# Optimization experiments

Measured on AMD Instinct MI355X. Metric: run time of the kernel, lower is better.

Reference implementation:

```python
import jax, jax.numpy as jnp
import numpy as np

B, S, H = 128, 1000, 256


def setup_inputs() -> dict:
    key = jax.random.key(0)
    ks = jax.random.split(key, 15)
    sc = 1.0 / np.sqrt(H)
    f = lambda k, shape: (jax.random.normal(k, shape, jnp.float32) * sc)
    return dict(
        static_hidden=jax.random.normal(ks[0], (B, S, H), jnp.float32),
        state_embedding=jax.random.normal(ks[1], (B, 1, H), jnp.float32),
        decoder_hidden=jax.random.normal(ks[2], (B, 1, H), jnp.float32),
        target_hidden=jax.random.normal(ks[3], (B, 1, H), jnp.float32),
        last_hh=jax.random.normal(ks[4], (1, B, H), jnp.float32),
        W_ih=f(ks[5], (3 * H, H)),
        W_hh=f(ks[6], (3 * H, H)),
        b_ih=f(ks[7], (3 * H,)),
        b_hh=f(ks[8], (3 * H,)),
        v_attn_enc=f(ks[9], (H,)),
        W_attn_enc=f(ks[10], (H, 2 * H)),
        v_attn_tgt=f(ks[11], (H,)),
        W_attn_tgt=f(ks[12], (H, 2 * H)),
        v_ptr=f(ks[13], (H,)),
        W_ptr=f(ks[14], (H, 3 * H)),
    )


def _attention(static, dec, v, W):
    # static: [B,S,H], dec: [B,1,H] -> softmax attention over S
    hid = jnp.concatenate([static, jnp.broadcast_to(dec, static.shape)], axis=2)  # [B,S,2H]
    t = jnp.tanh(jnp.einsum('hk,bsk->bhs', W, hid))  # [B,H,S]
    return jax.nn.softmax(jnp.einsum('h,bhs->bs', v, t), axis=1)  # [B,S]


def _gru_step(x, h, Wih, Whh, bih, bhh):
    # single-layer single-step torch GRU semantics; x,h: [B,H]
    gi = x @ Wih.T + bih
    gh = h @ Whh.T + bhh
    ir, iz, ig = jnp.split(gi, 3, axis=-1)
    hr, hz, hg = jnp.split(gh, 3, axis=-1)
    r = jax.nn.sigmoid(ir + hr)
    z = jax.nn.sigmoid(iz + hz)
    n = jnp.tanh(ig + r * hg)
    return (1.0 - z) * n + z * h


def _pointer_branch(static, state_emb, attn, v, W):
    context = jnp.einsum('bs,bsh->bh', attn, static)[:, None, :]  # [B,1,H]
    energy = jnp.concatenate(
        [static,
         jnp.broadcast_to(context, static.shape),
         jnp.broadcast_to(state_emb, static.shape)], axis=2)  # [B,S,3H]
    return jnp.einsum('h,bhs->bs', v, jnp.tanh(jnp.einsum('hk,bsk->bhs', W, energy)))


def reference(static_hidden, state_embedding, decoder_hidden, target_hidden, last_hh,
              W_ih, W_hh, b_ih, b_hh,
              v_attn_enc, W_attn_enc, v_attn_tgt, W_attn_tgt, v_ptr, W_ptr):
    # GRU step (dropout is identity in eval / p=0.0)
    h_new = _gru_step(decoder_hidden[:, 0, :], last_hh[0], W_ih, W_hh, b_ih, b_hh)
    rnn_out = h_new[:, None, :]  # [B,1,H]
    last_hh_new = h_new[None]    # [1,B,H]

    enc_attn = _attention(static_hidden, rnn_out, v_attn_enc, W_attn_enc)
    probs = _pointer_branch(static_hidden, state_embedding, enc_attn, v_ptr, W_ptr)

    tgt_attn = _attention(static_hidden, target_hidden, v_attn_tgt, W_attn_tgt)
    # NOTE: original code reuses self.v / self.W (not v_target/W_taret) for the
    # target branch energy -- replicated faithfully.
    probs_target = _pointer_branch(static_hidden, state_embedding, tgt_attn, v_ptr, W_ptr)

    return (5.0 * probs + probs_target, last_hh_new)
```

## Files before the change

### kernel.cpp

```cpp
#include <hip/hip_runtime.h>
#include <hip/hip_bf16.h>
#include <stdint.h>
#include <stddef.h>

#define Bn 128
#define Sn 1000
#define SP 1024
#define Hn 256

typedef __bf16 bf16;
typedef __bf16 bf16x8 __attribute__((ext_vector_type(8)));
typedef __bf16 bf16x4 __attribute__((ext_vector_type(4)));
typedef float  f32x16 __attribute__((ext_vector_type(16)));

typedef __attribute__((address_space(1))) const unsigned int* gas1;
typedef __attribute__((address_space(3))) unsigned int* las3;

__device__ __forceinline__ float fast_tanh(float x){
  return 1.0f - 2.0f / (__expf(2.0f * x) + 1.0f);
}
__device__ __forceinline__ float fast_sigmoid(float x){
  return 1.0f / (1.0f + __expf(-x));
}

__global__ void k0w(const float* __restrict__ We, const float* __restrict__ Wt,
                    const float* __restrict__ Wp, bf16* __restrict__ Wcb,
                    const float* __restrict__ dec, const float* __restrict__ lhh,
                    const float* __restrict__ tgt, const float* __restrict__ se,
                    float* __restrict__ xT, float* __restrict__ hT,
                    float* __restrict__ tT, float* __restrict__ sT){
  int blk = blockIdx.x, t = threadIdx.x;
  if (blk < 768){
    int tt = blk*256 + t;
    int r = tt >> 8, c = tt & 255;
    float val;
    if (r < 256)       val = We[r*512 + c];
    else if (r < 512)  val = Wt[(r-256)*512 + c];
    else               val = Wp[(r-512)*768 + c];
    Wcb[tt] = (bf16)val;
  } else {
    int idx = blk - 768;
    int a = idx >> 7, bb = idx & 127;
    const float* src = (a==0) ? dec : (a==1) ? lhh : (a==2) ? tgt : se;
    float* dst       = (a==0) ? xT  : (a==1) ? hT  : (a==2) ? tT  : sT;
    dst[t*128 + bb] = src[bb*256 + t];
  }
}

__global__ __launch_bounds__(512) void k1a_gru(
    const float* __restrict__ xT, const float* __restrict__ hT,
    const float* __restrict__ Wih, const float* __restrict__ Whh,
    const float* __restrict__ bih, const float* __restrict__ bhh,
    float* __restrict__ out_hh, float* __restrict__ hnT){
  int t = threadIdx.x;
  int g = t >> 7, b = t & 127;
  int h = blockIdx.x*4 + g;
  const float4* wir = (const float4*)(Wih + (size_t)h*256);
  const float4* wiz = (const float4*)(Wih + (size_t)(256+h)*256);
  const float4* wig = (const float4*)(Wih + (size_t)(512+h)*256);
  const float4* whr = (const float4*)(Whh + (size_t)h*256);
  const float4* whz = (const float4*)(Whh + (size_t)(256+h)*256);
  const float4* whg = (const float4*)(Whh + (size_t)(512+h)*256);
  float air=0.f, aiz=0.f, aig=0.f, ahr=0.f, ahz=0.f, ahg=0.f;
  #pragma unroll 2
  for (int kq=0; kq<64; kq++){
    float4 vir = wir[kq], viz = wiz[kq], vig = wig[kq];
    float4 vhr = whr[kq], vhz = whz[kq], vhg = whg[kq];
    #pragma unroll
    for (int e=0;e<4;e++){
      int k = kq*4 + e;
      float xv = xT[k*128 + b];
      float hv = hT[k*128 + b];
      air += (&vir.x)[e]*xv; aiz += (&viz.x)[e]*xv; aig += (&vig.x)[e]*xv;
      ahr += (&vhr.x)[e]*hv; ahz += (&vhz.x)[e]*hv; ahg += (&vhg.x)[e]*hv;
    }
  }
  air += bih[h];      ahr += bhh[h];
  aiz += bih[256+h];  ahz += bhh[256+h];
  aig += bih[512+h];  ahg += bhh[512+h];
  float r = fast_sigmoid(air + ahr);
  float z = fast_sigmoid(aiz + ahz);
  float n = fast_tanh(aig + r*ahg);
  float hprev = hT[h*128 + b];
  float hnew = (1.f - z)*n + z*hprev;
  out_hh[b*256 + h] = hnew;
  hnT[h*128 + b] = hnew;
}

__global__ __launch_bounds__(512) void k1c_dots(
    const float* __restrict__ hnT, const float* __restrict__ tT,
    const float* __restrict__ sT,
    const float* __restrict__ We, const float* __restrict__ Wt,
    const float* __restrict__ Wp,
    float* __restrict__ dEnc, float* __restrict__ dTgt, float* __restrict__ c3){
  int t = threadIdx.x;
  int g = t >> 7, b = t & 127;
  int vr = blockIdx.x*4 + g;
  int var = vr >> 8, h = vr & 255;
  const float* wrow; const float* X; float* dst;
  if (var == 0)      { wrow = We + (size_t)h*512 + 256; X = hnT; dst = dEnc; }
  else if (var == 1) { wrow = Wt + (size_t)h*512 + 256; X = tT;  dst = dTgt; }
  else               { wrow = Wp + (size_t)h*768 + 512; X = sT;  dst = c3; }
  const float4* w4 = (const float4*)wrow;
  float acc = 0.f;
  #pragma unroll 2
  for (int kq=0; kq<64; kq++){
    float4 wv = w4[kq];
    #pragma unroll
    for (int e=0;e<4;e++)
      acc += (&wv.x)[e] * X[(kq*4+e)*128 + b];
  }
  dst[b*256 + h] = acc;
}

__global__ __launch_bounds__(512) void k2_gemm(
    const float* __restrict__ stat, const bf16* __restrict__ Wcb,
    const float* __restrict__ dEnc, const float* __restrict__ dTgt,
    const float* __restrict__ vEnc, const float* __restrict__ vTgt,
    float* __restrict__ scE, float* __restrict__ scT, bf16* __restrict__ Aptr){
  __shared__ __align__(16) bf16 As[64*256];
  __shared__ __align__(16) bf16 Bs[256*64];
  __shared__ float pS[2][64];
  int tid = threadIdx.x, w = tid>>6, l = tid&63;
  int st = blockIdx.x, b = blockIdx.y;
  int wm = (w>>2)*32, wn = (w&3)*64;
  int l31 = l & 31, lh = l >> 5;
  if (tid < 128) pS[tid>>6][tid&63] = 0.f;

  #pragma unroll
  for (int is=0; is<8; is++){
    int fidx = is*512 + tid;
    int row = fidx >> 6, col4 = fidx & 63;
    int s = st*64 + row;
    float4 f = make_float4(0.f,0.f,0.f,0.f);
    if (s < Sn) f = ((const float4*)(stat + ((size_t)(b*Sn + s))*Hn))[col4];
    bf16x4 v;
    v[0]=(bf16)f.x; v[1]=(bf16)f.y; v[2]=(bf16)f.z; v[3]=(bf16)f.w;
    int c8 = col4 >> 1, half = col4 & 1;
    *(bf16x4*)(&As[row*256 + ((c8 ^ (row&7))<<3) + half*4]) = v;
  }

  for (int p=0; p<3; p++){
    f32x16 acc[2];
    #pragma unroll
    for (int j=0;j<2;j++)
      #pragma unroll
      for (int r=0;r<16;r++) acc[j][r] = 0.f;

    for (int kt=0; kt<4; kt++){
      __syncthreads();
      #pragma unroll
      for (int is=0; is<4; is++){
        int row = is*64 + w*8 + (l>>3);
        int gch = (l&7) ^ (row&7);
        __builtin_amdgcn_global_load_lds(
            (gas1)(Wcb + ((size_t)(p*256 + row))*256 + kt*64 + gch*8),
            (las3)(&Bs[(is*64 + w*8)*64]), 16, 0, 0);
      }
      __syncthreads();
      #pragma unroll
      for (int kc=0; kc<4; kc++){
        int rA = wm + l31;
        int ck = kt*8 + kc*2 + lh;
        bf16x8 af = *(const bf16x8*)(&As[rA*256 + ((ck ^ (rA&7))<<3)]);
        #pragma unroll
        for (int j=0;j<2;j++){
          int n = wn + j*32 + l31;
          int ckb = kc*2 + lh;
          bf16x8 bfv = *(const bf16x8*)(&Bs[n*64 + ((ckb ^ (n&7))<<3)]);
          acc[j] = __builtin_amdgcn_mfma_f32_32x32x16_bf16(af, bfv, acc[j], 0,0,0);
        }
      }
    }

    if (p < 2){
      const float* vv = p ? vTgt : vEnc;
      const float* db = (p ? dTgt : dEnc) + b*256;
      float vj[2], dj[2];
      #pragma unroll
      for (int j=0;j<2;j++){
        int hh = wn + j*32 + l31;
        vj[j] = vv[hh]; dj[j] = db[hh];
      }
      #pragma unroll
      for (int r=0;r<16;r++){
        float pp = vj[0]*fast_tanh(acc[0][r] + dj[0])
                 + vj[1]*fast_tanh(acc[1][r] + dj[1]);
        pp += __shfl_xor(pp,1); pp += __shfl_xor(pp,2);
        pp += __shfl_xor(pp,4); pp += __shfl_xor(pp,8); pp += __shfl_xor(pp,16);
        if (l31 == 0){
          int row = wm + (r&3) + 8*(r>>2) + 4*lh;
          atomicAdd(&pS[p][row], pp);
        }
      }
    } else {
      bf16* dst = Aptr + ((size_t)(b*16 + st))*16384;
      #pragma unroll
      for (int j=0;j<2;j++){
        #pragma unroll
        for (int q4=0;q4<4;q4++){
          bf16x4 v4;
          #pragma unroll
          for (int rr=0;rr<4;rr++) v4[rr] = (bf16)acc[j][q4*4+rr];
          int slot = w*8 + j*4 + q4;
          *(bf16x4*)(dst + ((size_t)(slot*64 + l))*4) = v4;
        }
      }
    }
  }
  __syncthreads();
  if (tid < 64)        scE[b*SP + st*64 + tid]      = pS[0][tid];
  else if (tid < 128)  scT[b*SP + st*64 + tid-64]   = pS[1][tid-64];
}

__global__ __launch_bounds__(1024) void k3_ctx(
    const float* __restrict__ scE, const float* __restrict__ scT,
    const float* __restrict__ stat, float* __restrict__ ctxG){
  __shared__ float attE[500], attT[500];
  __shared__ float redE[16], redT[16];
  __shared__ float4 pe4[16][64], pt4[16][64];
  int b = blockIdx.x, sg = blockIdx.y, t = threadIdx.x;
  int wid = t>>6, ln = t&63;

  float vE = (t < Sn) ? scE[b*SP + t] : -1e30f;
  float vT = (t < Sn) ? scT[b*SP + t] : -1e30f;
  float mE = vE, mT = vT;
  #pragma unroll
  for (int o=1;o<64;o<<=1){ mE=fmaxf(mE,__shfl_xor(mE,o)); mT=fmaxf(mT,__shfl_xor(mT,o)); }
  if (ln==0){ redE[wid]=mE; redT[wid]=mT; }
  __syncthreads();
  float ME=-1e30f, MT=-1e30f;
  #pragma unroll
  for (int i=0;i<16;i++){ ME=fmaxf(ME,redE[i]); MT=fmaxf(MT,redT[i]); }
  __syncthreads();
  float eE = (t < Sn) ? __expf(vE-ME) : 0.f;
  float eT = (t < Sn) ? __expf(vT-MT) : 0.f;
  float sE=eE, sT=eT;
  #pragma unroll
  for (int o=1;o<64;o<<=1){ sE+=__shfl_xor(sE,o); sT+=__shfl_xor(sT,o); }
  if (ln==0){ redE[wid]=sE; redT[wid]=sT; }
  __syncthreads();
  float SE=0.f, ST=0.f;
  #pragma unroll
  for (int i=0;i<16;i++){ SE+=redE[i]; ST+=redT[i]; }
  float invE = 1.f/SE, invT = 1.f/ST;
  if (t < 500){
    int s = sg*500 + t;
    attE[t] = __expf(scE[b*SP+s]-ME)*invE;
    attT[t] = __expf(scT[b*SP+s]-MT)*invT;
  }
  __syncthreads();

  int h4 = t & 63, rg = t >> 6;
  float4 aE = make_float4(0.f,0.f,0.f,0.f), aT = aE;
  int nrows = (rg == 15) ? 20 : 32;
  const float4* base = (const float4*)(stat + ((size_t)(b*Sn + sg*500 + rg*32))*Hn) + h4;
  #pragma unroll 4
  for (int i=0;i<nrows;i++){
    float4 f = base[(size_t)i*64];
    float wE = attE[rg*32 + i], wT = attT[rg*32 + i];
    aE.x += wE*f.x; aE.y += wE*f.y; aE.z += wE*f.z; aE.w += wE*f.w;
    aT.x += wT*f.x; aT.y += wT*f.y; aT.z += wT*f.z; aT.w += wT*f.w;
  }
  pe4[rg][h4] = aE; pt4[rg][h4] = aT;
  __syncthreads();
  if (t < 64){
    float4 s = make_float4(0.f,0.f,0.f,0.f);
    #pragma unroll
    for (int i=0;i<16;i++){
      float4 p = pe4[i][t];
      s.x+=p.x; s.y+=p.y; s.z+=p.z; s.w+=p.w;
    }
    atomicAdd(&ctxG[b*256 + t*4 + 0], s.x);
    atomicAdd(&ctxG[b*256 + t*4 + 1], s.y);
    atomicAdd(&ctxG[b*256 + t*4 + 2], s.z);
    atomicAdd(&ctxG[b*256 + t*4 + 3], s.w);
  } else if (t < 128){
    int h = t - 64;
    float4 s = make_float4(0.f,0.f,0.f,0.f);
    #pragma unroll
    for (int i=0;i<16;i++){
      float4 p = pt4[i][h];
      s.x+=p.x; s.y+=p.y; s.z+=p.z; s.w+=p.w;
    }
    atomicAdd(&ctxG[32768 + b*256 + h*4 + 0], s.x);
    atomicAdd(&ctxG[32768 + b*256 + h*4 + 1], s.y);
    atomicAdd(&ctxG[32768 + b*256 + h*4 + 2], s.z);
    atomicAdd(&ctxG[32768 + b*256 + h*4 + 3], s.w);
  }
}

__global__ __launch_bounds__(512) void k3c_c2(
    const float* __restrict__ ctxG, const float* __restrict__ Wp,
    const float* __restrict__ c3,
    float* __restrict__ cE, float* __restrict__ cT){
  __shared__ __align__(16) float ctxL[512];
  int b = blockIdx.x, t = threadIdx.x;
  ctxL[t] = ctxG[(t>>8)*32768 + b*256 + (t&255)];
  __syncthreads();
  int var = t >> 8, h = t & 255;
  const float4* w4 = (const float4*)(Wp + (size_t)h*768 + 256);
  const float4* cv = (const float4*)(&ctxL[var*256]);
  float acc = 0.f;
  #pragma unroll 4
  for (int k=0;k<64;k++){
    float4 wv = w4[k], xv = cv[k];
    acc += wv.x*xv.x + wv.y*xv.y + wv.z*xv.z + wv.w*xv.w;
  }
  (var ? cT : cE)[b*256 + h] = acc + c3[b*256 + h];
}

__global__ __launch_bounds__(512) void k4_final(
    const bf16* __restrict__ Aptr, const float* __restrict__ cE,
    const float* __restrict__ cT, const float* __restrict__ vp,
    float* __restrict__ out){
  __shared__ float pE[64], pT[64];
  int tid=threadIdx.x, w=tid>>6, l=tid&63;
  int st=blockIdx.x, b=blockIdx.y;
  int wm=(w>>2)*32, wn=(w&3)*64;
  int l31=l&31, lh=l>>5;
  if (tid < 128){ (tid<64 ? pE : pT)[tid&63] = 0.f; }
  __syncthreads();
  const bf16* src = Aptr + ((size_t)(b*16 + st))*16384;
  float vj[2], ej[2], tj[2];
  #pragma unroll
  for (int j=0;j<2;j++){
    int hh = wn + j*32 + l31;
    vj[j]=vp[hh]; ej[j]=cE[b*256+hh]; tj[j]=cT[b*256+hh];
  }
  float peR[16], ptR[16];
  #pragma unroll
  for (int r=0;r<16;r++){ peR[r]=0.f; ptR[r]=0.f; }
  #pragma unroll
  for (int j=0;j<2;j++){
    #pragma unroll
    for (int q4=0;q4<4;q4++){
      int slot = w*8 + j*4 + q4;
      bf16x4 v4 = *(const bf16x4*)(src + ((size_t)(slot*64 + l))*4);
      #pragma unroll
      for (int rr=0;rr<4;rr++){
        float a = (float)v4[rr];
        peR[q4*4+rr] += vj[j]*fast_tanh(a + ej[j]);
        ptR[q4*4+rr] += vj[j]*fast_tanh(a + tj[j]);
      }
    }
  }
  #pragma unroll
  for (int r=0;r<16;r++){
    float pe = peR[r], pt = ptR[r];
    pe += __shfl_xor(pe,1); pt += __shfl_xor(pt,1);
    pe += __shfl_xor(pe,2); pt += __shfl_xor(pt,2);
    pe += __shfl_xor(pe,4); pt += __shfl_xor(pt,4);
    pe += __shfl_xor(pe,8); pt += __shfl_xor(pt,8);
    pe += __shfl_xor(pe,16); pt += __shfl_xor(pt,16);
    if (l31 == 0){
      int row = wm + (r&3) + 8*(r>>2) + 4*lh;
      atomicAdd(&pE[row], pe);
      atomicAdd(&pT[row], pt);
    }
  }
  __syncthreads();
  if (tid < 64){
    int s = st*64 + tid;
    if (s < Sn) out[b*Sn + s] = 5.0f*pE[tid] + pT[tid];
  }
}

extern "C" void kernel_launch(void* const* d_in, const int* in_sizes, int n_in,
                              void* d_out, int out_size, void* d_ws, size_t ws_size,
                              hipStream_t stream){
  const float* stat = (const float*)d_in[0];
  const float* se   = (const float*)d_in[1];
  const float* dec  = (const float*)d_in[2];
  const float* tgt  = (const float*)d_in[3];
  const float* lhh  = (const float*)d_in[4];
  const float* Wih  = (const float*)d_in[5];
  const float* Whh  = (const float*)d_in[6];
  const float* bih  = (const float*)d_in[7];
  const float* bhh  = (const float*)d_in[8];
  const float* vEnc = (const float*)d_in[9];
  const float* WEnc = (const float*)d_in[10];
  const float* vTgt = (const float*)d_in[11];
  const float* WTgt = (const float*)d_in[12];
  const float* vPtr = (const float*)d_in[13];
  const float* WPtr = (const float*)d_in[14];
  float* out = (float*)d_out;

  char* wsp = (char*)d_ws;
  bf16*  Aptr = (bf16*)(wsp);
  bf16*  Wcb  = (bf16*)(wsp + 67108864);
  float* xT   = (float*)(wsp + 67502080);
  float* hT   = (float*)(wsp + 67633152);
  float* tT   = (float*)(wsp + 67764224);
  float* sT   = (float*)(wsp + 67895296);
  float* hnT  = (float*)(wsp + 68026368);
  float* scE  = (float*)(wsp + 68157440);
  float* scT  = (float*)(wsp + 68681728);
  float* dEnc = (float*)(wsp + 69206016);
  float* dTgt = (float*)(wsp + 69337088);
  float* c3   = (float*)(wsp + 69468160);
  float* cE   = (float*)(wsp + 69599232);
  float* cT   = (float*)(wsp + 69730304);
  float* ctxG = (float*)(wsp + 69861376);

  hipMemsetAsync(ctxG, 0, 262144, stream);
  hipLaunchKernelGGL(k0w, dim3(1280), dim3(256), 0, stream,
                     WEnc, WTgt, WPtr, Wcb, dec, lhh, tgt, se, xT, hT, tT, sT);
  hipLaunchKernelGGL(k1a_gru, dim3(64), dim3(512), 0, stream,
                     xT, hT, Wih, Whh, bih, bhh, out + Bn*Sn, hnT);
  hipLaunchKernelGGL(k1c_dots, dim3(192), dim3(512), 0, stream,
                     hnT, tT, sT, WEnc, WTgt, WPtr, dEnc, dTgt, c3);
  hipLaunchKernelGGL(k2_gemm, dim3(16, 128), dim3(512), 0, stream,
                     stat, Wcb, dEnc, dTgt, vEnc, vTgt, scE, scT, Aptr);
  hipLaunchKernelGGL(k3_ctx, dim3(128, 2), dim3(1024), 0, stream,
                     scE, scT, stat, ctxG);
  hipLaunchKernelGGL(k3c_c2, dim3(128), dim3(512), 0, stream,
                     ctxG, WPtr, c3, cE, cT);
  hipLaunchKernelGGL(k4_final, dim3(16, 128), dim3(512), 0, stream,
                     Aptr, cE, cT, vPtr, out);
}
```

Baseline: 450.4 us.

## Restructure k2 GEMM with double-buffered weight loads, pipelined A staging, row-major Aptr

k2_gemm drops to 256 threads. Each wave now computes a 64x64 tile with weights stationary, and the weight K-slices are double-buffered in LDS via async global-to-LDS loads, so the loads overlap the MFMA work. The static_hidden tile is converted to bf16 progressively during the first pass instead of in an up-front blocking loop. Score reductions move from shared atomics to per-lane register sums, and the pointer pre-activations are written row-major through LDS. k4_final is rewritten to read those contiguous rows with four threads per row, which trades more register pressure in k2 for fewer syncs and more coalesced stores.

```diff
diff --git a/kernel.cpp b/kernel.cpp
--- a/kernel.cpp
+++ b/kernel.cpp
@@ -113,104 +113,155 @@
   dst[b*256 + h] = acc;
 }
 
-__global__ __launch_bounds__(512) void k2_gemm(
+__global__ __launch_bounds__(256) void k2_gemm(
     const float* __restrict__ stat, const bf16* __restrict__ Wcb,
     const float* __restrict__ dEnc, const float* __restrict__ dTgt,
     const float* __restrict__ vEnc, const float* __restrict__ vTgt,
     float* __restrict__ scE, float* __restrict__ scT, bf16* __restrict__ Aptr){
   __shared__ __align__(16) bf16 As[64*256];
-  __shared__ __align__(16) bf16 Bs[256*64];
-  __shared__ float pS[2][64];
+  __shared__ __align__(16) bf16 Bs[2][256*32];
   int tid = threadIdx.x, w = tid>>6, l = tid&63;
+  int l31 = l&31, lh = l>>5;
   int st = blockIdx.x, b = blockIdx.y;
-  int wm = (w>>2)*32, wn = (w&3)*64;
-  int l31 = l & 31, lh = l >> 5;
-  if (tid < 128) pS[tid>>6][tid&63] = 0.f;
-
-  #pragma unroll
-  for (int is=0; is<8; is++){
-    int fidx = is*512 + tid;
-    int row = fidx >> 6, col4 = fidx & 63;
-    int s = st*64 + row;
-    float4 f = make_float4(0.f,0.f,0.f,0.f);
-    if (s < Sn) f = ((const float4*)(stat + ((size_t)(b*Sn + s))*Hn))[col4];
-    bf16x4 v;
-    v[0]=(bf16)f.x; v[1]=(bf16)f.y; v[2]=(bf16)f.z; v[3]=(bf16)f.w;
-    int c8 = col4 >> 1, half = col4 & 1;
-    *(bf16x4*)(&As[row*256 + ((c8 ^ (row&7))<<3) + half*4]) = v;
-  }
-
+
+  int am = tid>>2, agk = tid&3;
+  bool aValid = (st*64 + am) < Sn;
+  const float4* aSrc4 = (const float4*)(stat + ((size_t)b*Sn + st*64 + am)*Hn);
+
+  int bnb = w*16 + (l>>2);
+  int bg  = l&3;
+
+  float4 pl0 = make_float4(0.f,0.f,0.f,0.f), pl1 = pl0;
+  if (aValid){ pl0 = aSrc4[agk*2]; pl1 = aSrc4[agk*2+1]; }
+  #pragma unroll
+  for (int i=0;i<4;i++){
+    int n = i*64 + bnb;
+    int g = bg ^ ((n>>1)&3);
+    __builtin_amdgcn_global_load_lds((gas1)(Wcb + (size_t)n*256 + g*8),
+                                     (las3)(&Bs[0][i*2048 + w*512]), 16, 0, 0);
+  }
+  {
+    bf16x8 v;
+    v[0]=(bf16)pl0.x; v[1]=(bf16)pl0.y; v[2]=(bf16)pl0.z; v[3]=(bf16)pl0.w;
+    v[4]=(bf16)pl1.x; v[5]=(bf16)pl1.y; v[6]=(bf16)pl1.z; v[7]=(bf16)pl1.w;
+    *(bf16x8*)&As[am*256 + ((agk ^ (am&7))<<3)] = v;
+  }
+  __syncthreads();
+
+  float scp0[2] = {0.f, 0.f}, scp1[2] = {0.f, 0.f};
+
+  #pragma unroll
   for (int p=0; p<3; p++){
-    f32x16 acc[2];
-    #pragma unroll
-    for (int j=0;j<2;j++)
+    f32x16 acc[2][2];
+    #pragma unroll
+    for (int a=0;a<2;a++)
       #pragma unroll
-      for (int r=0;r<16;r++) acc[j][r] = 0.f;
-
-    for (int kt=0; kt<4; kt++){
-      __syncthreads();
+      for (int c=0;c<2;c++)
+        #pragma unroll
+        for (int r=0;r<16;r++) acc[a][c][r] = 0.f;
+
+    #pragma unroll
+    for (int kt=0; kt<8; kt++){
+      int it = p*8 + kt;
+      float4 q0 = make_float4(0.f,0.f,0.f,0.f), q1 = q0;
+      bool doA = (p==0) && (kt<7);
+      if (doA && aValid){ q0 = aSrc4[(kt+1)*8 + agk*2]; q1 = aSrc4[(kt+1)*8 + agk*2 + 1]; }
+      if (it < 23){
+        int itn = it+1, pn = itn>>3, ktn = itn&7;
+        const bf16* wb = Wcb + (size_t)pn*65536 + ktn*32;
+        bf16* ldsb = &Bs[(it&1)^1][0];
+        #pragma unroll
+        for (int i=0;i<4;i++){
+          int n = i*64 + bnb;
+          int g = bg ^ ((n>>1)&3);
+          __builtin_amdgcn_global_load_lds((gas1)(wb + (size_t)n*256 + g*8),
+                                           (las3)(ldsb + i*2048 + w*512), 16, 0, 0);
+        }
+      }
+      const bf16* bsr = &Bs[it&1][0];
       #pragma unroll
-      for (int is=0; is<4; is++){
-        int row = is*64 + w*8 + (l>>3);
-        int gch = (l&7) ^ (row&7);
-        __builtin_amdgcn_global_load_lds(
-            (gas1)(Wcb + ((size_t)(p*256 + row))*256 + kt*64 + gch*8),
-            (las3)(&Bs[(is*64 + w*8)*64]), 16, 0, 0);
+      for (int ks=0; ks<2; ks++){
+        int kg = ks*2 + lh;
+        int swzA = ((kt*4 + kg) ^ (l31&7))<<3;
+        bf16x8 af0 = *(const bf16x8*)&As[l31*256 + swzA];
+        bf16x8 af1 = *(const bf16x8*)&As[(32+l31)*256 + swzA];
+        #pragma unroll
+        for (int c=0;c<2;c++){
+          int n = w*64 + c*32 + l31;
+          bf16x8 wf = *(const bf16x8*)&bsr[n*32 + ((kg ^ ((n>>1)&3))<<3)];
+          acc[0][c] = __builtin_amdgcn_mfma_f32_32x32x16_bf16(wf, af0, acc[0][c], 0,0,0);
+          acc[1][c] = __builtin_amdgcn_mfma_f32_32x32x16_bf16(wf, af1, acc[1][c], 0,0,0);
+        }
+      }
+      if (doA){
+        bf16x8 v;
+        v[0]=(bf16)q0.x; v[1]=(bf16)q0.y; v[2]=(bf16)q0.z; v[3]=(bf16)q0.w;
+        v[4]=(bf16)q1.x; v[5]=(bf16)q1.y; v[6]=(bf16)q1.z; v[7]=(bf16)q1.w;
+        int G = (kt+1)*4 + agk;
+        *(bf16x8*)&As[am*256 + ((G ^ (am&7))<<3)] = v;
       }
       __syncthreads();
-      #pragma unroll
-      for (int kc=0; kc<4; kc++){
-        int rA = wm + l31;
-        int ck = kt*8 + kc*2 + lh;
-        bf16x8 af = *(const bf16x8*)(&As[rA*256 + ((ck ^ (rA&7))<<3)]);
-        #pragma unroll
-        for (int j=0;j<2;j++){
-          int n = wn + j*32 + l31;
-          int ckb = kc*2 + lh;
-          bf16x8 bfv = *(const bf16x8*)(&Bs[n*64 + ((ckb ^ (n&7))<<3)]);
-          acc[j] = __builtin_amdgcn_mfma_f32_32x32x16_bf16(af, bfv, acc[j], 0,0,0);
-        }
-      }
     }
 
     if (p < 2){
       const float* vv = p ? vTgt : vEnc;
       const float* db = (p ? dTgt : dEnc) + b*256;
-      float vj[2], dj[2];
+      float s0 = 0.f, s1 = 0.f;
       #pragma unroll
-      for (int j=0;j<2;j++){
-        int hh = wn + j*32 + l31;
-        vj[j] = vv[hh]; dj[j] = db[hh];
-      }
-      #pragma unroll
-      for (int r=0;r<16;r++){
-        float pp = vj[0]*fast_tanh(acc[0][r] + dj[0])
-                 + vj[1]*fast_tanh(acc[1][r] + dj[1]);
-        pp += __shfl_xor(pp,1); pp += __shfl_xor(pp,2);
-        pp += __shfl_xor(pp,4); pp += __shfl_xor(pp,8); pp += __shfl_xor(pp,16);
-        if (l31 == 0){
-          int row = wm + (r&3) + 8*(r>>2) + 4*lh;
-          atomicAdd(&pS[p][row], pp);
+      for (int c=0;c<2;c++){
+        int nb = w*64 + c*32 + 4*lh;
+        #pragma unroll
+        for (int r=0;r<16;r++){
+          int n = nb + (r&3) + 8*(r>>2);
+          float vdv = vv[n], ddv = db[n];
+          s0 += vdv * fast_tanh(acc[0][c][r] + ddv);
+          s1 += vdv * fast_tanh(acc[1][c][r] + ddv);
         }
       }
+      scp0[p] = s0; scp1[p] = s1;
     } else {
-      bf16* dst = Aptr + ((size_t)(b*16 + st))*16384;
       #pragma unroll
-      for (int j=0;j<2;j++){
+      for (int a=0;a<2;a++){
+        int m = a*32 + l31;
         #pragma unroll
-        for (int q4=0;q4<4;q4++){
-          bf16x4 v4;
+        for (int c=0;c<2;c++){
+          int g0 = w*8 + c*4 + lh*2;
+          bf16x8 lo, hi;
           #pragma unroll
-          for (int rr=0;rr<4;rr++) v4[rr] = (bf16)acc[j][q4*4+rr];
-          int slot = w*8 + j*4 + q4;
-          *(bf16x4*)(dst + ((size_t)(slot*64 + l))*4) = v4;
+          for (int r=0;r<8;r++){ lo[r] = (bf16)acc[a][c][r]; hi[r] = (bf16)acc[a][c][8+r]; }
+          *(bf16x8*)&As[m*256 + (( g0    ^ (m&7))<<3)] = lo;
+          *(bf16x8*)&As[m*256 + (((g0+1) ^ (m&7))<<3)] = hi;
         }
       }
     }
   }
-  __syncthreads();
-  if (tid < 64)        scE[b*SP + st*64 + tid]      = pS[0][tid];
-  else if (tid < 128)  scT[b*SP + st*64 + tid-64]   = pS[1][tid-64];
+
+  float* scr = (float*)&Bs[0][0];
+  #pragma unroll
+  for (int p2=0;p2<2;p2++){
+    float v0 = scp0[p2] + __shfl_xor(scp0[p2], 32);
+    float v1 = scp1[p2] + __shfl_xor(scp1[p2], 32);
+    if (lh == 0){
+      scr[(p2*4 + w)*64 + l31]      = v0;
+      scr[(p2*4 + w)*64 + 32 + l31] = v1;
+    }
+  }
+  __syncthreads();
+  if (tid < 128){
+    int pp = tid>>6, m = tid&63;
+    float s = scr[pp*256 + m] + scr[pp*256 + 64 + m]
+            + scr[pp*256 + 128 + m] + scr[pp*256 + 192 + m];
+    (pp ? scT : scE)[b*SP + st*64 + m] = s;
+  }
+  {
+    int m = tid>>2, part = tid&3;
+    bf16* dst = Aptr + ((size_t)(b*1024 + st*64 + m))*256 + part*64;
+    #pragma unroll
+    for (int i=0;i<8;i++){
+      int g = (part*8 + i) ^ (m&7);
+      *(bf16x8*)(dst + i*8) = *(const bf16x8*)&As[m*256 + (g<<3)];
+    }
+  }
 }
 
 __global__ __launch_bounds__(1024) void k3_ctx(
@@ -310,60 +361,42 @@
   (var ? cT : cE)[b*256 + h] = acc + c3[b*256 + h];
 }
 
-__global__ __launch_bounds__(512) void k4_final(
+__global__ __launch_bounds__(256) void k4_final(
     const bf16* __restrict__ Aptr, const float* __restrict__ cE,
     const float* __restrict__ cT, const float* __restrict__ vp,
     float* __restrict__ out){
-  __shared__ float pE[64], pT[64];
-  int tid=threadIdx.x, w=tid>>6, l=tid&63;
-  int st=blockIdx.x, b=blockIdx.y;
-  int wm=(w>>2)*32, wn=(w&3)*64;
-  int l31=l&31, lh=l>>5;
-  if (tid < 128){ (tid<64 ? pE : pT)[tid&63] = 0.f; }
-  __syncthreads();
-  const bf16* src = Aptr + ((size_t)(b*16 + st))*16384;
-  float vj[2], ej[2], tj[2];
-  #pragma unroll
-  for (int j=0;j<2;j++){
-    int hh = wn + j*32 + l31;
-    vj[j]=vp[hh]; ej[j]=cE[b*256+hh]; tj[j]=cT[b*256+hh];
-  }
-  float peR[16], ptR[16];
-  #pragma unroll
-  for (int r=0;r<16;r++){ peR[r]=0.f; ptR[r]=0.f; }
-  #pragma unroll
-  for (int j=0;j<2;j++){
-    #pragma unroll
-    for (int q4=0;q4<4;q4++){
-      int slot = w*8 + j*4 + q4;
-      bf16x4 v4 = *(const bf16x4*)(src + ((size_t)(slot*64 + l))*4);
-      #pragma unroll
-      for (int rr=0;rr<4;rr++){
-        float a = (float)v4[rr];
-        peR[q4*4+rr] += vj[j]*fast_tanh(a + ej[j]);
-        ptR[q4*4+rr] += vj[j]*fast_tanh(a + tj[j]);
-      }
-    }
-  }
-  #pragma unroll
-  for (int r=0;r<16;r++){
-    float pe = peR[r], pt = ptR[r];
-    pe += __shfl_xor(pe,1); pt += __shfl_xor(pt,1);
-    pe += __shfl_xor(pe,2); pt += __shfl_xor(pt,2);
-    pe += __shfl_xor(pe,4); pt += __shfl_xor(pt,4);
-    pe += __shfl_xor(pe,8); pt += __shfl_xor(pt,8);
-    pe += __shfl_xor(pe,16); pt += __shfl_xor(pt,16);
-    if (l31 == 0){
-      int row = wm + (r&3) + 8*(r>>2) + 4*lh;
-      atomicAdd(&pE[row], pe);
-      atomicAdd(&pT[row], pt);
-    }
-  }
-  __syncthreads();
-  if (tid < 64){
-    int s = st*64 + tid;
-    if (s < Sn) out[b*Sn + s] = 5.0f*pE[tid] + pT[tid];
-  }
+  int t = threadIdx.x;
+  int st = blockIdx.x, b = blockIdx.y;
+  int m = t>>2, part = t&3;
+  const bf16* src = Aptr + ((size_t)(b*1024 + st*64 + m))*256 + part*64;
+  const float* vpb = vp + part*64;
+  const float* ceb = cE + b*256 + part*64;
+  const float* ctb = cT + b*256 + part*64;
+  float pe = 0.f, pt = 0.f;
+  #pragma unroll
+  for (int i=0;i<8;i++){
+    bf16x8 av = *(const bf16x8*)(src + i*8);
+    int bi = ((i>>2)<<5) + (((i>>1)&1)<<2) + ((i&1)<<4);
+    float4 v0 = *(const float4*)(vpb + bi), v1 = *(const float4*)(vpb + bi + 8);
+    float4 e0 = *(const float4*)(ceb + bi), e1 = *(const float4*)(ceb + bi + 8);
+    float4 t0 = *(const float4*)(ctb + bi), t1 = *(const float4*)(ctb + bi + 8);
+    #pragma unroll
+    for (int j=0;j<4;j++){
+      float a = (float)av[j];
+      pe += (&v0.x)[j] * fast_tanh(a + (&e0.x)[j]);
+      pt += (&v0.x)[j] * fast_tanh(a + (&t0.x)[j]);
+    }
+    #pragma unroll
+    for (int j=0;j<4;j++){
+      float a = (float)av[4+j];
+      pe += (&v1.x)[j] * fast_tanh(a + (&e1.x)[j]);
+      pt += (&v1.x)[j] * fast_tanh(a + (&t1.x)[j]);
+    }
+  }
+  pe += __shfl_xor(pe,1); pe += __shfl_xor(pe,2);
+  pt += __shfl_xor(pt,1); pt += __shfl_xor(pt,2);
+  int s = st*64 + m;
+  if (part==0 && s < Sn) out[(size_t)b*Sn + s] = 5.0f*pe + pt;
 }
 
 extern "C" void kernel_launch(void* const* d_in, const int* in_sizes, int n_in,
@@ -410,12 +443,12 @@
                      xT, hT, Wih, Whh, bih, bhh, out + Bn*Sn, hnT);
   hipLaunchKernelGGL(k1c_dots, dim3(192), dim3(512), 0, stream,
                      hnT, tT, sT, WEnc, WTgt, WPtr, dEnc, dTgt, c3);
-  hipLaunchKernelGGL(k2_gemm, dim3(16, 128), dim3(512), 0, stream,
+  hipLaunchKernelGGL(k2_gemm, dim3(16, 128), dim3(256), 0, stream,
                      stat, Wcb, dEnc, dTgt, vEnc, vTgt, scE, scT, Aptr);
   hipLaunchKernelGGL(k3_ctx, dim3(128, 2), dim3(1024), 0, stream,
                      scE, scT, stat, ctxG);
   hipLaunchKernelGGL(k3c_c2, dim3(128), dim3(512), 0, stream,
                      ctxG, WPtr, c3, cE, cT);
-  hipLaunchKernelGGL(k4_final, dim3(16, 128), dim3(512), 0, stream,
+  hipLaunchKernelGGL(k4_final, dim3(16, 128), dim3(256), 0, stream,
                      Aptr, cE, cT, vPtr, out);
 }
```

Result: slower. 464.1 us (+3.1%).
